# Kernel optimization log

Hardware: AMD Instinct MI355X
Metric: run time of the kernel (lower is better)

The kernel has to match this reference:

```python
import jax, jax.numpy as jnp
import numpy as np

HIDDEN = 4096
N_HEADS = 32
N_KV_HEADS = 8
HEAD_DIM = HIDDEN // N_HEADS  # 128
N_GROUPS = N_HEADS // N_KV_HEADS  # 4
ROPE_THETA = 10000.0
BSZ, SEQ = 2, 2048


def rotate_half(x):
    x1 = x[..., : x.shape[-1] // 2]
    x2 = x[..., x.shape[-1] // 2 :]
    return jnp.concatenate((-x2, x1), axis=-1)


def rope_tables(seq_len, head_dim, theta):
    inv_freq = 1.0 / theta ** (jnp.arange(0, head_dim, 2, dtype=jnp.float32) / head_dim)
    t = jnp.arange(seq_len, dtype=jnp.float32)
    freqs = jnp.einsum('i,j->ij', t, inv_freq)          # [S, head_dim/2]
    emb = jnp.concatenate((freqs, freqs), axis=-1)       # [S, head_dim]
    return jnp.cos(emb), jnp.sin(emb)


def setup_inputs() -> dict:
    key = jax.random.key(0)
    ks = jax.random.split(key, 5)
    hidden_states = jax.random.normal(ks[0], (BSZ, SEQ, HIDDEN), dtype=jnp.float32)
    # causal additive mask [B, 1, Q, K]
    causal = jnp.tril(jnp.ones((SEQ, SEQ), dtype=bool))
    attention_mask = jnp.where(causal, 0.0, -1e9).astype(jnp.float32)
    attention_mask = jnp.broadcast_to(attention_mask[None, None], (BSZ, 1, SEQ, SEQ))
    position_ids = jnp.broadcast_to(jnp.arange(SEQ, dtype=jnp.int32)[None, :], (BSZ, SEQ))
    sc = 1.0 / np.sqrt(HIDDEN)
    Wq = jax.random.normal(ks[1], (HIDDEN, N_HEADS * HEAD_DIM), dtype=jnp.float32) * sc
    Wk = jax.random.normal(ks[2], (HIDDEN, N_KV_HEADS * HEAD_DIM), dtype=jnp.float32) * sc
    Wv = jax.random.normal(ks[3], (HIDDEN, N_KV_HEADS * HEAD_DIM), dtype=jnp.float32) * sc
    Wo = jax.random.normal(ks[4], (N_HEADS * HEAD_DIM, HIDDEN), dtype=jnp.float32) * sc
    return {
        'hidden_states': hidden_states,
        'attention_mask': attention_mask,
        'position_ids': position_ids,
        'Wq': Wq, 'Wk': Wk, 'Wv': Wv, 'Wo': Wo,
    }


def reference(hidden_states, attention_mask, position_ids, Wq, Wk, Wv, Wo):
    bsz, q_len, _ = hidden_states.shape
    # QKV projections
    q = (hidden_states @ Wq).reshape(bsz, q_len, N_HEADS, HEAD_DIM).swapaxes(1, 2)       # [B,H,S,D]
    k = (hidden_states @ Wk).reshape(bsz, q_len, N_KV_HEADS, HEAD_DIM).swapaxes(1, 2)    # [B,Hkv,S,D]
    v = (hidden_states @ Wv).reshape(bsz, q_len, N_KV_HEADS, HEAD_DIM).swapaxes(1, 2)    # [B,Hkv,S,D]
    # RoPE
    cos_t, sin_t = rope_tables(q_len, HEAD_DIM, ROPE_THETA)
    cos = jnp.take(cos_t, position_ids, axis=0)[:, None]  # [B,1,S,D]
    sin = jnp.take(sin_t, position_ids, axis=0)[:, None]
    q = q * cos + rotate_half(q) * sin
    k = k * cos + rotate_half(k) * sin
    # GQA attention via grouped einsum (equivalent to repeat_kv, without materializing repeats)
    qg = q.reshape(bsz, N_KV_HEADS, N_GROUPS, q_len, HEAD_DIM)
    scores = jnp.einsum('bhgqd,bhkd->bhgqk', qg, k) / jnp.sqrt(jnp.float32(HEAD_DIM))
    scores = scores + attention_mask[:, :, None]  # broadcast mask over (kv_head, group)
    probs = jax.nn.softmax(scores.astype(jnp.float32), axis=-1).astype(hidden_states.dtype)
    out = jnp.einsum('bhgqk,bhkd->bhgqd', probs, v)
    out = out.reshape(bsz, N_HEADS, q_len, HEAD_DIM).swapaxes(1, 2).reshape(bsz, q_len, HIDDEN)
    return out @ Wo
```

## Files before the change

kernel.cpp:

```cpp
#include <hip/hip_runtime.h>
#include <hip/hip_bf16.h>
#include <cstdint>

#define HIDDEN 4096
#define NH 32
#define NKV 8
#define HD 128
#define SEQ 2048
#define BSZ 2
#define QKVN 6144
#define QKVLD 6144

using bf16x8 = __attribute__((ext_vector_type(8))) short;
using f32x4  = __attribute__((ext_vector_type(4))) float;
using f32x16 = __attribute__((ext_vector_type(16))) float;

__device__ __forceinline__ ushort f2bf(float f) {
  union { float f; uint32_t u; } v; v.f = f;
  uint32_t r = (v.u + 0x7FFFu + ((v.u >> 16) & 1u)) >> 16;
  return (ushort)r;
}
__device__ __forceinline__ float bf2f(ushort s) {
  union { uint32_t u; float f; } v; v.u = ((uint32_t)s) << 16;
  return v.f;
}

__device__ __forceinline__ uint32_t cvtpk(float lo, float hi) {
  uint32_t r;
  asm("v_cvt_pk_bf16_f32 %0, %1, %2" : "=v"(r) : "v"(lo), "v"(hi));
  return r;
}
__device__ __forceinline__ void pl32swap(uint32_t& a, uint32_t& b) {
  asm("v_permlane32_swap_b32 %0, %1" : "+v"(a), "+v"(b));
}

__device__ __forceinline__ void gload_lds16(const void* g, void* l) {
  __builtin_amdgcn_global_load_lds(
      (const __attribute__((address_space(1))) void*)g,
      (__attribute__((address_space(3))) void*)l, 16, 0, 0);
}

__global__ __launch_bounds__(256)
void cvt_bf16_kernel(const float* __restrict__ X, ushort* __restrict__ Xb, int n8) {
  int t = blockIdx.x * 256 + threadIdx.x;
  if (t >= n8) return;
  size_t i = (size_t)t * 8;
  float4 a = *(const float4*)(X + i);
  float4 b = *(const float4*)(X + i + 4);
  uint4 p;
  p.x = (uint)f2bf(a.x) | ((uint)f2bf(a.y) << 16);
  p.y = (uint)f2bf(a.z) | ((uint)f2bf(a.w) << 16);
  p.z = (uint)f2bf(b.x) | ((uint)f2bf(b.y) << 16);
  p.w = (uint)f2bf(b.z) | ((uint)f2bf(b.w) << 16);
  *(uint4*)(Xb + i) = p;
}

__global__ __launch_bounds__(256)
void transpose_all_kernel(const float* __restrict__ Wq, const float* __restrict__ Wk,
                          const float* __restrict__ Wv, const float* __restrict__ Wo,
                          ushort* __restrict__ BTqkv, ushort* __restrict__ WoT) {
  __shared__ ushort tile[64][72];
  const int id = blockIdx.x;
  const float* W; ushort* WT; int N, rel;
  if (id < 4096)      { W = Wq; WT = BTqkv;                          N = 4096; rel = id; }
  else if (id < 5120) { W = Wk; WT = BTqkv + (size_t)4096 * 4096;    N = 1024; rel = id - 4096; }
  else if (id < 6144) { W = Wv; WT = BTqkv + (size_t)5120 * 4096;    N = 1024; rel = id - 5120; }
  else                { W = Wo; WT = WoT;                            N = 4096; rel = id - 6144; }
  const int K = 4096;
  const int nb = N >> 6;
  const int n0 = (rel % nb) * 64, k0 = (rel / nb) * 64;

  const int tr = threadIdx.x >> 4;
  const int tc = (threadIdx.x & 15) * 4;
#pragma unroll
  for (int i = 0; i < 4; ++i) {
    const int k = tr + i * 16;
    float4 v = *(const float4*)(W + (size_t)(k0 + k) * N + n0 + tc);
    ushort4 u;
    u.x = f2bf(v.x); u.y = f2bf(v.y); u.z = f2bf(v.z); u.w = f2bf(v.w);
    *(ushort4*)&tile[k][tc] = u;
  }
  __syncthreads();
  const int nr = threadIdx.x >> 3;
  const int kc = (threadIdx.x & 7) * 8;
#pragma unroll
  for (int i = 0; i < 2; ++i) {
    const int n = nr + i * 32;
    bf16x8 o;
#pragma unroll
    for (int j = 0; j < 8; ++j) o[j] = tile[kc + j][n];
    *(bf16x8*)(WT + (size_t)(n0 + n) * K + k0 + kc) = o;
  }
}

__global__ __launch_bounds__(256)
void transpose_v_kernel(const ushort* __restrict__ Vsrc, ushort* __restrict__ VtG) {
  __shared__ ushort tile[64][72];
  const int slice = blockIdx.z;
  const int b = slice >> 3, kh = slice & 7;
  const int s0 = blockIdx.x * 64, d0 = blockIdx.y * 64;
  const ushort* src = Vsrc + ((size_t)(b * SEQ) + s0) * QKVLD + kh * HD + d0;
  const int sr = threadIdx.x >> 3;
  const int dc = (threadIdx.x & 7) * 8;
#pragma unroll
  for (int i = 0; i < 2; ++i) {
    const int s = sr + i * 32;
    *(bf16x8*)&tile[s][dc] = *(const bf16x8*)(src + (size_t)s * QKVLD + dc);
  }
  __syncthreads();
  ushort* dst = VtG + ((size_t)slice * HD + d0) * SEQ + s0;
  const int dr = threadIdx.x >> 3;
  const int sc = (threadIdx.x & 7) * 8;
#pragma unroll
  for (int i = 0; i < 2; ++i) {
    const int d = dr + i * 32;
    bf16x8 o;
#pragma unroll
    for (int j = 0; j < 8; ++j) o[j] = tile[sc + j][d];
    *(bf16x8*)(dst + (size_t)d * SEQ + sc) = o;
  }
}

__global__ __launch_bounds__(512, 2)
void gemmqkv_kernel(const ushort* __restrict__ A, const ushort* __restrict__ BT,
                    ushort* __restrict__ Cp, int M, int N, int K) {
  extern __shared__ ushort lds[];
  const int tid = threadIdx.x, lane = tid & 63, wave = tid >> 6;
  const int l15 = lane & 15, l4 = lane >> 4;
  const int wr = wave >> 2, wc = wave & 3;

  const int mt = M >> 8, ntile = N / 192, nwg = mt * ntile;
  const int swq = nwg >> 3, swr = nwg & 7;
  const int xcd = blockIdx.x & 7, lo = blockIdx.x >> 3;
  const int wg = (xcd < swr ? xcd * (swq + 1) : swr * (swq + 1) + (xcd - swr) * swq) + lo;
  const int m0 = (wg % mt) << 8;
  const int n0 = (wg / mt) * 192;

  ushort* LA[2][2];
  ushort* LB[2][2];
#pragma unroll
  for (int b_ = 0; b_ < 2; ++b_)
#pragma unroll
    for (int s_ = 0; s_ < 2; ++s_) {
      LA[b_][s_] = lds + (b_ * 2 + s_) * 8192;
      LB[b_][s_] = lds + 32768 + (b_ * 2 + s_) * 6144;
    }

  const ushort* Abase = A + (size_t)m0 * K;
  const ushort* Bbase = BT + (size_t)n0 * K;

  const int srow0 = tid >> 2;
  const int scol8 = (((tid & 3) ^ ((srow0 >> 1) & 3)) << 3);
  const int bs1 = tid;
  const int brow1 = bs1 >> 2;
  const int bcol1 = (((bs1 & 3) ^ ((bs1 >> 3) & 3)) << 3);
  const int bs2 = 512 + wave * 32 + (lane & 31);
  const int brow2 = bs2 >> 2;
  const int bcol2 = (((bs2 & 3) ^ ((bs2 >> 3) & 3)) << 3);

  const int swb  = (l4 ^ ((l15 >> 1) & 3)) << 3;
  const int aoff = (wr * 128 + l15) * 32 + swb;
  const int boff = (wc * 48 + l15) * 32 + swb;

  f32x4 acc[8][3] = {};
  bf16x8 a[4];
  bf16x8 b[3];

#define STAGE_EV(buf, ks, kt)                                                  \
  do {                                                                         \
    const size_t gc_ = (size_t)(kt) * 64 + (ks) * 32;                          \
    gload_lds16(Abase + (size_t)srow0 * K + gc_ + scol8,                       \
                &LA[buf][ks][tid * 8]);                                        \
    gload_lds16(Bbase + (size_t)brow1 * K + gc_ + bcol1,                       \
                &LB[buf][ks][tid * 8]);                                        \
  } while (0)

#define STAGE_OD(buf, ks, kt)                                                  \
  do {                                                                         \
    const size_t gc_ = (size_t)(kt) * 64 + (ks) * 32;                          \
    gload_lds16(Abase + (size_t)(128 + srow0) * K + gc_ + scol8,               \
                &LA[buf][ks][(512 + tid) * 8]);                                \
    if ((lane & 32) == 0)                                                      \
      gload_lds16(Bbase + (size_t)brow2 * K + gc_ + bcol2,                     \
                  &LB[buf][ks][(512 + wave * 32 + (lane & 31)) * 8]);          \
  } while (0)

#define MFMA_ __builtin_amdgcn_mfma_f32_16x16x32_bf16

#define PHASE_EVEN(buf, ks, sb, sk, skt)                                       \
  {                                                                            \
    _Pragma("unroll") for (int m_ = 0; m_ < 4; ++m_)                           \
      a[m_] = *(const bf16x8*)&LA[buf][ks][aoff + m_ * 512];                   \
    _Pragma("unroll") for (int n_ = 0; n_ < 3; ++n_)                           \
      b[n_] = *(const bf16x8*)&LB[buf][ks][boff + n_ * 512];                   \
    STAGE_EV(sb, sk, skt);                                                     \
    asm volatile("s_barrier" ::: "memory");                                    \
    __builtin_amdgcn_s_setprio(1);                                             \
    _Pragma("unroll") for (int m_ = 0; m_ < 4; ++m_)                           \
      _Pragma("unroll") for (int n_ = 0; n_ < 3; ++n_)                         \
        acc[m_][n_] = MFMA_(a[m_], b[n_], acc[m_][n_], 0, 0, 0);               \
    __builtin_amdgcn_s_setprio(0);                                             \
    asm volatile("s_barrier" ::: "memory");                                    \
  }

#define PHASE_ODD(buf, ks, sb, sk, skt)                                        \
  {                                                                            \
    _Pragma("unroll") for (int m_ = 0; m_ < 4; ++m_)                           \
      a[m_] = *(const bf16x8*)&LA[buf][ks][aoff + (4 + m_) * 512];             \
    STAGE_OD(sb, sk, skt);                                                     \
    asm volatile("s_barrier" ::: "memory");                                    \
    __builtin_amdgcn_s_setprio(1);                                             \
    _Pragma("unroll") for (int m_ = 0; m_ < 4; ++m_)                           \
      _Pragma("unroll") for (int n_ = 0; n_ < 3; ++n_)                         \
        acc[4 + m_][n_] = MFMA_(a[m_], b[n_], acc[4 + m_][n_], 0, 0, 0);       \
    __builtin_amdgcn_s_setprio(0);                                             \
    asm volatile("s_waitcnt vmcnt(8)");                                        \
    asm volatile("s_barrier" ::: "memory");                                    \
  }

  const int NT = K >> 6;

  STAGE_EV(0, 0, 0); STAGE_OD(0, 0, 0);
  STAGE_EV(0, 1, 0); STAGE_OD(0, 1, 0);
  STAGE_EV(1, 0, 1); STAGE_OD(1, 0, 1);
  asm volatile("s_waitcnt vmcnt(8)");
  asm volatile("s_barrier" ::: "memory");

  for (int i = 0; i < (NT >> 1); ++i) {
    const int kt0 = 2 * i;
    const int ktA = (kt0 + 2 < NT) ? kt0 + 2 : NT - 1;
    const int ktB = (kt0 + 3 < NT) ? kt0 + 3 : NT - 1;
    PHASE_EVEN(0, 0, 1, 1, kt0 + 1)
    PHASE_ODD (0, 0, 1, 1, kt0 + 1)
    PHASE_EVEN(0, 1, 0, 0, ktA)
    PHASE_ODD (0, 1, 0, 0, ktA)
    PHASE_EVEN(1, 0, 0, 1, ktA)
    PHASE_ODD (1, 0, 0, 1, ktA)
    PHASE_EVEN(1, 1, 1, 0, ktB)
    PHASE_ODD (1, 1, 1, 0, ktB)
  }
#undef PHASE_EVEN
#undef PHASE_ODD
#undef STAGE_EV
#undef STAGE_OD

  const int crow0 = m0 + wr * 128 + l4 * 4;
  const int ccol0 = n0 + wc * 48 + l15;
#pragma unroll
  for (int m_ = 0; m_ < 8; ++m_)
#pragma unroll
    for (int n_ = 0; n_ < 3; ++n_)
#pragma unroll
      for (int r_ = 0; r_ < 4; ++r_) {
        const size_t row = crow0 + m_ * 16 + r_;
        const int col = ccol0 + n_ * 16;
        Cp[row * N + col] = f2bf(acc[m_][n_][r_]);
      }
}

template<int OUT_BF16>
__global__ __launch_bounds__(512, 2)
void gemm8p_kernel(const ushort* __restrict__ A, const ushort* __restrict__ BT,
                   void* __restrict__ Cp, int M, int N, int K) {
  extern __shared__ ushort lds[];
  const int tid = threadIdx.x, lane = tid & 63, wave = tid >> 6;
  const int l15 = lane & 15, l4 = lane >> 4;
  const int wr = wave >> 2, wc = wave & 3;

  const int mt = M >> 8, nt = N >> 8, nwg = mt * nt;
  const int swq = nwg >> 3, swr = nwg & 7;
  const int xcd = blockIdx.x & 7, lo = blockIdx.x >> 3;
  const int wg = (xcd < swr ? xcd * (swq + 1) : swr * (swq + 1) + (xcd - swr) * swq) + lo;
  const int m0 = (wg % mt) << 8;
  const int n0 = (wg / mt) << 8;

  ushort* LA[2][2];
  ushort* LB[2][2];
#pragma unroll
  for (int b_ = 0; b_ < 2; ++b_)
#pragma unroll
    for (int s_ = 0; s_ < 2; ++s_) {
      LA[b_][s_] = lds + ((b_ * 2 + 0) * 2 + s_) * 8192;
      LB[b_][s_] = lds + ((b_ * 2 + 1) * 2 + s_) * 8192;
    }

  const ushort* Abase = A + (size_t)m0 * K;
  const ushort* Bbase = BT + (size_t)n0 * K;

  const int srow0 = tid >> 2;
  const int scol8 = (((tid & 3) ^ ((srow0 >> 1) & 3)) << 3);

  const int swb  = (l4 ^ ((l15 >> 1) & 3)) << 3;
  const int aoff = (wr * 128 + l15) * 32 + swb;
  const int boff = (wc * 64 + l15) * 32 + swb;

  f32x4 acc[8][4] = {};
  bf16x8 a[8];
  bf16x8 b[4];

#define STAGE(buf, ks, kt, part)                                              \
  do {                                                                        \
    const size_t gc_ = (size_t)(kt) * 64 + (ks) * 32 + scol8;                 \
    const int rw_ = srow0 + (part) * 128;                                     \
    const int dst_ = ((part) * 512 + tid) * 8;                                \
    gload_lds16(Abase + (size_t)rw_ * K + gc_, &LA[buf][ks][dst_]);           \
    gload_lds16(Bbase + (size_t)rw_ * K + gc_, &LB[buf][ks][dst_]);           \
  } while (0)

#define MFMA_ __builtin_amdgcn_mfma_f32_16x16x32_bf16

#define PHASE_EVEN(buf, ks, sb, sk, skt)                                      \
  {                                                                           \
    _Pragma("unroll") for (int m_ = 0; m_ < 8; ++m_)                          \
      a[m_] = *(const bf16x8*)&LA[buf][ks][aoff + m_ * 512];                  \
    b[0] = *(const bf16x8*)&LB[buf][ks][boff];                                \
    b[1] = *(const bf16x8*)&LB[buf][ks][boff + 512];                          \
    STAGE(sb, sk, skt, 0);                                                    \
    asm volatile("s_barrier" ::: "memory");                                   \
    __builtin_amdgcn_s_setprio(1);                                            \
    _Pragma("unroll") for (int m_ = 0; m_ < 8; ++m_) {                        \
      acc[m_][0] = MFMA_(a[m_], b[0], acc[m_][0], 0, 0, 0);                   \
      acc[m_][1] = MFMA_(a[m_], b[1], acc[m_][1], 0, 0, 0);                   \
    }                                                                         \
    __builtin_amdgcn_s_setprio(0);                                            \
    asm volatile("s_barrier" ::: "memory");                                   \
  }

#define PHASE_ODD(buf, ks, sb, sk, skt)                                       \
  {                                                                           \
    b[2] = *(const bf16x8*)&LB[buf][ks][boff + 1024];                         \
    b[3] = *(const bf16x8*)&LB[buf][ks][boff + 1536];                         \
    STAGE(sb, sk, skt, 1);                                                    \
    asm volatile("s_barrier" ::: "memory");                                   \
    __builtin_amdgcn_s_setprio(1);                                            \
    _Pragma("unroll") for (int m_ = 0; m_ < 8; ++m_) {                        \
      acc[m_][2] = MFMA_(a[m_], b[2], acc[m_][2], 0, 0, 0);                   \
      acc[m_][3] = MFMA_(a[m_], b[3], acc[m_][3], 0, 0, 0);                   \
    }                                                                         \
    __builtin_amdgcn_s_setprio(0);                                            \
    asm volatile("s_waitcnt vmcnt(8)");                                       \
    asm volatile("s_barrier" ::: "memory");                                   \
  }

  const int NT = K >> 6;

  STAGE(0, 0, 0, 0); STAGE(0, 0, 0, 1);
  STAGE(0, 1, 0, 0); STAGE(0, 1, 0, 1);
  STAGE(1, 0, 1, 0); STAGE(1, 0, 1, 1);
  asm volatile("s_waitcnt vmcnt(8)");
  asm volatile("s_barrier" ::: "memory");

  for (int i = 0; i < (NT >> 1); ++i) {
    const int kt0 = 2 * i;
    const int ktA = (kt0 + 2 < NT) ? kt0 + 2 : NT - 1;
    const int ktB = (kt0 + 3 < NT) ? kt0 + 3 : NT - 1;
    PHASE_EVEN(0, 0, 1, 1, kt0 + 1)
    PHASE_ODD (0, 0, 1, 1, kt0 + 1)
    PHASE_EVEN(0, 1, 0, 0, ktA)
    PHASE_ODD (0, 1, 0, 0, ktA)
    PHASE_EVEN(1, 0, 0, 1, ktA)
    PHASE_ODD (1, 0, 0, 1, ktA)
    PHASE_EVEN(1, 1, 1, 0, ktB)
    PHASE_ODD (1, 1, 1, 0, ktB)
  }
#undef PHASE_EVEN
#undef PHASE_ODD
#undef STAGE

  const int crow0 = m0 + wr * 128 + l4 * 4;
  const int ccol0 = n0 + wc * 64 + l15;
#pragma unroll
  for (int m_ = 0; m_ < 8; ++m_)
#pragma unroll
    for (int n_ = 0; n_ < 4; ++n_)
#pragma unroll
      for (int r_ = 0; r_ < 4; ++r_) {
        const size_t row = crow0 + m_ * 16 + r_;
        const int col = ccol0 + n_ * 16;
        const float val = acc[m_][n_][r_];
        if (OUT_BF16) ((ushort*)Cp)[row * N + col] = f2bf(val);
        else          ((float*)Cp)[row * N + col]  = val;
      }
}

__global__ __launch_bounds__(256)
void rope_qk_kernel(ushort* qkv, const int* __restrict__ pos_ids, int total) {
  int t = blockIdx.x * 256 + threadIdx.x;
  if (t >= total) return;
  int j = t & 63;
  int rest = t >> 6;
  int hp = rest % 40;
  int bs = rest / 40;
  float pos = (float)pos_ids[bs];
  float inv = exp2f(-(float)j * (13.287712379549449f / 64.0f));
  float ang = pos * inv;
  const float osc = (hp < 32) ? 0.12751731f : 1.0f;
  float c = cosf(ang) * osc, s = sinf(ang) * osc;
  const int col = (hp < 32) ? hp * HD : HIDDEN + (hp - 32) * HD;
  ushort* p = qkv + (size_t)bs * QKVLD + col + j;
  float x1 = bf2f(p[0]), x2 = bf2f(p[64]);
  p[0]  = f2bf(x1 * c - x2 * s);
  p[64] = f2bf(x2 * c + x1 * s);
}

__global__ __launch_bounds__(512)
void attn_kernel(const ushort* __restrict__ Q, const ushort* __restrict__ K0,
                 const ushort* __restrict__ VtG, ushort* __restrict__ AO) {
  extern __shared__ ushort alds[];
  ushort* Ks[4];
  ushort* Vs[4];
#pragma unroll
  for (int i = 0; i < 4; ++i) {
    Ks[i] = alds + i * 8192;
    Vs[i] = alds + 32768 + i * 8192;
  }

  const int bid = blockIdx.x;
  const int kh  = bid & 7;
  const int r2  = bid >> 3;
  const int qtB = 7 - (r2 & 7);
  const int hq  = (r2 >> 3) & 3;
  const int b   = r2 >> 5;
  const int h   = kh * 4 + hq;
  const int q0b = qtB * 256;

  const int tid = threadIdx.x, lane = tid & 63, w = tid >> 6;
  const int l31 = lane & 31, hi = lane >> 5;
  const int q0w = q0b + w * 32;

  const size_t bS = (size_t)b * SEQ;
  const ushort* Kb = K0 + bS * QKVLD + kh * HD;
  const ushort* Vb = VtG + (size_t)(b * NKV + kh) * HD * SEQ;

  bf16x8 qf[8];
  {
    const ushort* qp = Q + (bS + q0w + l31) * QKVLD + h * HD + hi * 8;
#pragma unroll
    for (int ds = 0; ds < 8; ++ds) qf[ds] = *(const bf16x8*)(qp + ds * 16);
  }

  f32x16 accO[4] = {};
  float mrow = -1e30f, denom = 0.0f;

  const int nt = qtB * 4 + 4;

  const int j0 = 2 * w, j1 = 2 * w + 1;
  const int kl4 = lane >> 4, ks15 = lane & 15;
  const int vl3 = lane >> 3, vs7 = lane & 7;
  const int kswz = lane & 15;
  const int vswz = lane & 7;

#define KSTAGE(jj, bb, kk0) { const int k_ = (jj) * 4 + kl4;                   \
    gload_lds16(Kb + (size_t)((kk0) + k_) * QKVLD + ((ks15 ^ (k_ & 15)) << 3), \
                &Ks[bb][(jj) * 512 + lane * 8]); }
#define VSTAGE(jj, bb, kk0) { const int d_ = (jj) * 8 + vl3;                   \
    gload_lds16(Vb + (size_t)d_ * SEQ + (kk0) + ((vs7 ^ (d_ & 7)) << 3),       \
                &Vs[bb][(jj) * 512 + lane * 8]); }

  KSTAGE(j0, 0, 0)  KSTAGE(j1, 0, 0)  VSTAGE(j0, 0, 0)  VSTAGE(j1, 0, 0)
  KSTAGE(j0, 1, 64) KSTAGE(j1, 1, 64) VSTAGE(j0, 1, 64) VSTAGE(j1, 1, 64)
  __syncthreads();

  for (int t = 0; t < nt; t += 2) {
    if (t + 2 < nt) {
      const int bb = (t + 2) & 3, kk = (t + 2) * 64;
      KSTAGE(j0, bb, kk) KSTAGE(j1, bb, kk) VSTAGE(j0, bb, kk) VSTAGE(j1, bb, kk)
    }
    if (t + 3 < nt) {
      const int bb = (t + 3) & 3, kk = (t + 3) * 64;
      KSTAGE(j0, bb, kk) KSTAGE(j1, bb, kk) VSTAGE(j0, bb, kk) VSTAGE(j1, bb, kk)
    }

#pragma unroll
    for (int u = 0; u < 2; ++u) {
      const int tt = t + u;
      const int k0 = tt * 64;
      const int cb = tt & 3;
      if (k0 > q0w + 31) continue;

      f32x16 s0 = {}, s1 = {};
      __builtin_amdgcn_s_setprio(1);
#pragma unroll
      for (int ds = 0; ds < 8; ++ds) {
        const int so = ((ds * 2 + hi) ^ kswz) << 3;
        bf16x8 kf0 = *(const bf16x8*)&Ks[cb][l31 * 128 + so];
        bf16x8 kf1 = *(const bf16x8*)&Ks[cb][(32 + l31) * 128 + so];
        s0 = __builtin_amdgcn_mfma_f32_32x32x16_bf16(kf0, qf[ds], s0, 0, 0, 0);
        s1 = __builtin_amdgcn_mfma_f32_32x32x16_bf16(kf1, qf[ds], s1, 0, 0, 0);
      }
      __builtin_amdgcn_s_setprio(0);

      if (k0 + 63 > q0w) {
        const int qrel = q0w + l31 - k0;
#pragma unroll
        for (int r = 0; r < 16; ++r) {
          const int kc = (r & 3) + 8 * (r >> 2) + 4 * hi;
          if (kc > qrel)      s0[r] = -1e30f;
          if (kc + 32 > qrel) s1[r] = -1e30f;
        }
      }
      float pm = s0[0];
#pragma unroll
      for (int r = 1; r < 16; ++r) pm = fmaxf(pm, s0[r]);
#pragma unroll
      for (int r = 0; r < 16; ++r) pm = fmaxf(pm, s1[r]);

      if (!__all(pm - mrow <= 8.0f)) {
        pm = fmaxf(pm, __shfl_xor(pm, 32));
        const float mn = fmaxf(mrow, pm);
        const float alpha = exp2f(mrow - mn);
        mrow = mn;
        denom *= alpha;
#pragma unroll
        for (int du = 0; du < 4; ++du)
#pragma unroll
          for (int r = 0; r < 16; ++r) accO[du][r] *= alpha;
      }
      float ssum = 0.0f;
#pragma unroll
      for (int r = 0; r < 16; ++r) { float p = exp2f(s0[r] - mrow); s0[r] = p; ssum += p; }
#pragma unroll
      for (int r = 0; r < 16; ++r) { float p = exp2f(s1[r] - mrow); s1[r] = p; ssum += p; }
      denom += ssum;

      uint32_t paw[4][4];
      {
        uint32_t p0 = cvtpk(s0[0], s0[1]),   p1 = cvtpk(s0[2], s0[3]);
        uint32_t p2 = cvtpk(s0[4], s0[5]),   p3 = cvtpk(s0[6], s0[7]);
        uint32_t p4 = cvtpk(s0[8], s0[9]),   p5 = cvtpk(s0[10], s0[11]);
        uint32_t p6 = cvtpk(s0[12], s0[13]), p7 = cvtpk(s0[14], s0[15]);
        pl32swap(p0, p2); pl32swap(p1, p3); pl32swap(p4, p6); pl32swap(p5, p7);
        paw[0][0] = p0; paw[0][1] = p1; paw[0][2] = p2; paw[0][3] = p3;
        paw[1][0] = p4; paw[1][1] = p5; paw[1][2] = p6; paw[1][3] = p7;
      }
      {
        uint32_t p0 = cvtpk(s1[0], s1[1]),   p1 = cvtpk(s1[2], s1[3]);
        uint32_t p2 = cvtpk(s1[4], s1[5]),   p3 = cvtpk(s1[6], s1[7]);
        uint32_t p4 = cvtpk(s1[8], s1[9]),   p5 = cvtpk(s1[10], s1[11]);
        uint32_t p6 = cvtpk(s1[12], s1[13]), p7 = cvtpk(s1[14], s1[15]);
        pl32swap(p0, p2); pl32swap(p1, p3); pl32swap(p4, p6); pl32swap(p5, p7);
        paw[2][0] = p0; paw[2][1] = p1; paw[2][2] = p2; paw[2][3] = p3;
        paw[3][0] = p4; paw[3][1] = p5; paw[3][2] = p6; paw[3][3] = p7;
      }

      __builtin_amdgcn_s_setprio(1);
#pragma unroll
      for (int du = 0; du < 4; ++du) {
#pragma unroll
        for (int ks = 0; ks < 4; ++ks) {
          const int so = ((ks * 2 + hi) ^ vswz) << 3;
          bf16x8 vf = *(const bf16x8*)&Vs[cb][(du * 32 + l31) * 64 + so];
          bf16x8 pb = *(const bf16x8*)&paw[ks][0];
          accO[du] = __builtin_amdgcn_mfma_f32_32x32x16_bf16(vf, pb, accO[du], 0, 0, 0);
        }
      }
      __builtin_amdgcn_s_setprio(0);
    }
    __syncthreads();
  }
#undef KSTAGE
#undef VSTAGE

  denom += __shfl_xor(denom, 32);
  const float inv = 1.0f / denom;
  ushort* op = AO + (bS + q0w + l31) * HIDDEN + h * HD + hi * 4;
#pragma unroll
  for (int du = 0; du < 4; ++du)
#pragma unroll
    for (int g = 0; g < 4; ++g) {
      uint2 u;
      u.x = cvtpk(accO[du][4 * g + 0] * inv, accO[du][4 * g + 1] * inv);
      u.y = cvtpk(accO[du][4 * g + 2] * inv, accO[du][4 * g + 3] * inv);
      *(uint2*)(op + du * 32 + g * 8) = u;
    }
}

extern "C" void kernel_launch(void* const* d_in, const int* in_sizes, int n_in,
                              void* d_out, int out_size, void* d_ws, size_t ws_size,
                              hipStream_t stream) {
  (void)in_sizes; (void)n_in; (void)out_size; (void)ws_size;
  const float* X   = (const float*)d_in[0];
  const int*   pos = (const int*)d_in[2];
  const float* Wq  = (const float*)d_in[3];
  const float* Wk  = (const float*)d_in[4];
  const float* Wv  = (const float*)d_in[5];
  const float* Wo  = (const float*)d_in[6];

  char* ws = (char*)d_ws;
  ushort* Xb    = (ushort*)(ws);
  ushort* QKV   = (ushort*)(ws + 33554432);
  ushort* BTqkv = (ushort*)(ws + 83886080);
  ushort* WoT   = (ushort*)(ws + 134217728);
  ushort* AO    = Xb;
  ushort* VtG   = BTqkv;

  const int M = BSZ * SEQ;
  dim3 blk(256);

  hipFuncSetAttribute((const void*)gemmqkv_kernel,
                      hipFuncAttributeMaxDynamicSharedMemorySize, 114688);
  hipFuncSetAttribute((const void*)gemm8p_kernel<0>,
                      hipFuncAttributeMaxDynamicSharedMemorySize, 131072);
  hipFuncSetAttribute((const void*)attn_kernel,
                      hipFuncAttributeMaxDynamicSharedMemorySize, 131072);

  cvt_bf16_kernel<<<dim3((M * HIDDEN / 8 + 255) / 256), blk, 0, stream>>>(X, Xb, M * HIDDEN / 8);
  transpose_all_kernel<<<dim3(10240), blk, 0, stream>>>(Wq, Wk, Wv, Wo, BTqkv, WoT);

  gemmqkv_kernel<<<dim3((M / 256) * (QKVN / 192)), dim3(512), 114688, stream>>>(
      Xb, BTqkv, QKV, M, QKVN, HIDDEN);

  rope_qk_kernel<<<dim3((M * 40 * 64) / 256), blk, 0, stream>>>(QKV, pos, M * 40 * 64);
  transpose_v_kernel<<<dim3(SEQ / 64, HD / 64, BSZ * NKV), blk, 0, stream>>>(
      QKV + HIDDEN + NKV * HD, VtG);

  attn_kernel<<<dim3(512), dim3(512), 131072, stream>>>(QKV, QKV + HIDDEN, VtG, AO);

  gemm8p_kernel<0><<<dim3((M / 256) * (HIDDEN / 256)), dim3(512), 131072, stream>>>(
      AO, WoT, d_out, M, HIDDEN, HIDDEN);
}
```

Measured before the change: 569.6 us.

## Halve attention query tile to 128 rows with double-buffered K/V staging

The attention kernel now runs 1024 blocks of 256 threads, each covering 128 query rows instead of 256. K/V staging drops from a 4-deep ring to a double buffer, so LDS use falls from 128KB to 64KB. Each warp now stages four rows instead of two, and the loop processes one 64-key tile per iteration with a barrier after each. The goal is more resident blocks per CU, better causal load balance and less wasted work. The cost is a shallower prefetch, more barriers per key, and each K/V tile being loaded by twice as many blocks.

```diff
diff --git a/kernel.cpp b/kernel.cpp
--- a/kernel.cpp
+++ b/kernel.cpp
@@ -403,26 +403,26 @@
   p[64] = f2bf(x2 * c + x1 * s);
 }
 
-__global__ __launch_bounds__(512)
+__global__ __launch_bounds__(256)
 void attn_kernel(const ushort* __restrict__ Q, const ushort* __restrict__ K0,
                  const ushort* __restrict__ VtG, ushort* __restrict__ AO) {
   extern __shared__ ushort alds[];
-  ushort* Ks[4];
-  ushort* Vs[4];
-#pragma unroll
-  for (int i = 0; i < 4; ++i) {
+  ushort* Ks[2];
+  ushort* Vs[2];
+#pragma unroll
+  for (int i = 0; i < 2; ++i) {
     Ks[i] = alds + i * 8192;
-    Vs[i] = alds + 32768 + i * 8192;
+    Vs[i] = alds + 16384 + i * 8192;
   }
 
   const int bid = blockIdx.x;
   const int kh  = bid & 7;
   const int r2  = bid >> 3;
-  const int qtB = 7 - (r2 & 7);
-  const int hq  = (r2 >> 3) & 3;
-  const int b   = r2 >> 5;
+  const int qtB = 15 - (r2 & 15);
+  const int hq  = (r2 >> 4) & 3;
+  const int b   = r2 >> 6;
   const int h   = kh * 4 + hq;
-  const int q0b = qtB * 256;
+  const int q0b = qtB * 128;
 
   const int tid = threadIdx.x, lane = tid & 63, w = tid >> 6;
   const int l31 = lane & 31, hi = lane >> 5;
@@ -442,9 +442,8 @@
   f32x16 accO[4] = {};
   float mrow = -1e30f, denom = 0.0f;
 
-  const int nt = qtB * 4 + 4;
-
-  const int j0 = 2 * w, j1 = 2 * w + 1;
+  const int nt = qtB * 2 + 2;
+
   const int kl4 = lane >> 4, ks15 = lane & 15;
   const int vl3 = lane >> 3, vs7 = lane & 7;
   const int kswz = lane & 15;
@@ -456,35 +455,31 @@
 #define VSTAGE(jj, bb, kk0) { const int d_ = (jj) * 8 + vl3;                   \
     gload_lds16(Vb + (size_t)d_ * SEQ + (kk0) + ((vs7 ^ (d_ & 7)) << 3),       \
                 &Vs[bb][(jj) * 512 + lane * 8]); }
-
-  KSTAGE(j0, 0, 0)  KSTAGE(j1, 0, 0)  VSTAGE(j0, 0, 0)  VSTAGE(j1, 0, 0)
-  KSTAGE(j0, 1, 64) KSTAGE(j1, 1, 64) VSTAGE(j0, 1, 64) VSTAGE(j1, 1, 64)
+#define KSTAGE4(bb, kk0) { KSTAGE(4*w, bb, kk0) KSTAGE(4*w+1, bb, kk0)         \
+                           KSTAGE(4*w+2, bb, kk0) KSTAGE(4*w+3, bb, kk0) }
+#define VSTAGE4(bb, kk0) { VSTAGE(4*w, bb, kk0) VSTAGE(4*w+1, bb, kk0)         \
+                           VSTAGE(4*w+2, bb, kk0) VSTAGE(4*w+3, bb, kk0) }
+
+  KSTAGE4(0, 0) VSTAGE4(0, 0)
   __syncthreads();
 
-  for (int t = 0; t < nt; t += 2) {
-    if (t + 2 < nt) {
-      const int bb = (t + 2) & 3, kk = (t + 2) * 64;
-      KSTAGE(j0, bb, kk) KSTAGE(j1, bb, kk) VSTAGE(j0, bb, kk) VSTAGE(j1, bb, kk)
+  for (int t = 0; t < nt; ++t) {
+    const int k0 = t * 64;
+    const int cur = t & 1;
+
+    if (t + 1 < nt) {
+      const int kn = k0 + 64;
+      KSTAGE4(cur ^ 1, kn) VSTAGE4(cur ^ 1, kn)
     }
-    if (t + 3 < nt) {
-      const int bb = (t + 3) & 3, kk = (t + 3) * 64;
-      KSTAGE(j0, bb, kk) KSTAGE(j1, bb, kk) VSTAGE(j0, bb, kk) VSTAGE(j1, bb, kk)
-    }
-
-#pragma unroll
-    for (int u = 0; u < 2; ++u) {
-      const int tt = t + u;
-      const int k0 = tt * 64;
-      const int cb = tt & 3;
-      if (k0 > q0w + 31) continue;
-
+
+    if (k0 <= q0w + 31) {
       f32x16 s0 = {}, s1 = {};
       __builtin_amdgcn_s_setprio(1);
 #pragma unroll
       for (int ds = 0; ds < 8; ++ds) {
         const int so = ((ds * 2 + hi) ^ kswz) << 3;
-        bf16x8 kf0 = *(const bf16x8*)&Ks[cb][l31 * 128 + so];
-        bf16x8 kf1 = *(const bf16x8*)&Ks[cb][(32 + l31) * 128 + so];
+        bf16x8 kf0 = *(const bf16x8*)&Ks[cur][l31 * 128 + so];
+        bf16x8 kf1 = *(const bf16x8*)&Ks[cur][(32 + l31) * 128 + so];
         s0 = __builtin_amdgcn_mfma_f32_32x32x16_bf16(kf0, qf[ds], s0, 0, 0, 0);
         s1 = __builtin_amdgcn_mfma_f32_32x32x16_bf16(kf1, qf[ds], s1, 0, 0, 0);
       }
@@ -549,7 +544,7 @@
 #pragma unroll
         for (int ks = 0; ks < 4; ++ks) {
           const int so = ((ks * 2 + hi) ^ vswz) << 3;
-          bf16x8 vf = *(const bf16x8*)&Vs[cb][(du * 32 + l31) * 64 + so];
+          bf16x8 vf = *(const bf16x8*)&Vs[cur][(du * 32 + l31) * 64 + so];
           bf16x8 pb = *(const bf16x8*)&paw[ks][0];
           accO[du] = __builtin_amdgcn_mfma_f32_32x32x16_bf16(vf, pb, accO[du], 0, 0, 0);
         }
@@ -560,6 +555,8 @@
   }
 #undef KSTAGE
 #undef VSTAGE
+#undef KSTAGE4
+#undef VSTAGE4
 
   denom += __shfl_xor(denom, 32);
   const float inv = 1.0f / denom;
@@ -602,7 +599,7 @@
   hipFuncSetAttribute((const void*)gemm8p_kernel<0>,
                       hipFuncAttributeMaxDynamicSharedMemorySize, 131072);
   hipFuncSetAttribute((const void*)attn_kernel,
-                      hipFuncAttributeMaxDynamicSharedMemorySize, 131072);
+                      hipFuncAttributeMaxDynamicSharedMemorySize, 65536);
 
   cvt_bf16_kernel<<<dim3((M * HIDDEN / 8 + 255) / 256), blk, 0, stream>>>(X, Xb, M * HIDDEN / 8);
   transpose_all_kernel<<<dim3(10240), blk, 0, stream>>>(Wq, Wk, Wv, Wo, BTqkv, WoT);
@@ -614,7 +611,7 @@
   transpose_v_kernel<<<dim3(SEQ / 64, HD / 64, BSZ * NKV), blk, 0, stream>>>(
       QKV + HIDDEN + NKV * HD, VtG);
 
-  attn_kernel<<<dim3(512), dim3(512), 131072, stream>>>(QKV, QKV + HIDDEN, VtG, AO);
+  attn_kernel<<<dim3(1024), dim3(256), 65536, stream>>>(QKV, QKV + HIDDEN, VtG, AO);
 
   gemm8p_kernel<0><<<dim3((M / 256) * (HIDDEN / 256)), dim3(512), 131072, stream>>>(
       AO, WoT, d_out, M, HIDDEN, HIDDEN);
```

Result: slower. 648.9 us (+13.9%).
